# Kernel tuning notes

Measured on AMD Instinct MI355X. Metric: run time of the kernel, lower is better.

## Reference

```python
import jax, jax.numpy as jnp
import numpy as np

B, T, H, W, C = 8, 32, 64, 64, 3
F = 24        # conv filters
U = 128       # lstm units
O = 1         # output units

def _conv(x, w, b):
    # x: [N,H,W,Cin], w: [3,3,Cin,Cout], SAME padding, linear activation
    y = jax.lax.conv_general_dilated(x, w, window_strides=(1, 1), padding='SAME',
                                     dimension_numbers=('NHWC', 'HWIO', 'NHWC'))
    return y + b

def setup_inputs() -> dict:
    key = jax.random.key(0)
    ks = jax.random.split(key, 16)
    s = lambda *shape: 0.05
    inp = {
        'x': jax.random.normal(ks[0], (B, T, H, W, C), dtype=jnp.float32),
        'conv1_w': jax.random.normal(ks[1], (3, 3, C, F), dtype=jnp.float32) * 0.1,
        'conv1_b': jnp.zeros((F,), jnp.float32),
        'conv2_w': jax.random.normal(ks[2], (3, 3, F, F), dtype=jnp.float32) * 0.1,
        'conv2_b': jnp.zeros((F,), jnp.float32),
        'Wf': jax.random.normal(ks[3], (F + U, U), dtype=jnp.float32) * 0.08,
        'bf': jnp.zeros((U,), jnp.float32),
        'Wi': jax.random.normal(ks[4], (F + U, U), dtype=jnp.float32) * 0.08,
        'bi': jnp.zeros((U,), jnp.float32),
        'Wc': jax.random.normal(ks[5], (F + U, U), dtype=jnp.float32) * 0.08,
        'bc': jnp.zeros((U,), jnp.float32),
        'Wo': jax.random.normal(ks[6], (F + U, U), dtype=jnp.float32) * 0.08,
        'bo': jnp.zeros((U,), jnp.float32),
        'out_w': jax.random.normal(ks[7], (U, O), dtype=jnp.float32) * 0.08,
        'out_b': jnp.zeros((O,), jnp.float32),
    }
    return inp

def reference(x, conv1_w, conv1_b, conv2_w, conv2_b, Wf, bf, Wi, bi, Wc, bc, Wo, bo, out_w, out_b):
    b, t, h, w, c = x.shape
    # CNN block (per-frame): two linear 3x3 convs, no pooling inside block
    xr = x.reshape(b * t, h, w, c)
    xr = _conv(xr, conv1_w, conv1_b)
    xr = _conv(xr, conv2_w, conv2_b)
    # TimeDistributed(GlobalAvgPool2D): mean over H,W -> [B,T,F]
    feat = xr.reshape(b, t, h, w, -1).mean(axis=(2, 3))

    # custom LSTM recurrence over time via scan
    def step(carry, xt):
        hs, cs = carry
        z = jnp.concatenate([xt, hs], axis=-1)           # [B, F+U]
        f = jax.nn.sigmoid(z @ Wf + bf)
        i = jax.nn.sigmoid(z @ Wi + bi)
        g = jnp.tanh(z @ Wc + bc)
        o = jax.nn.sigmoid(z @ Wo + bo)
        c_new = cs * f + i * g
        h_new = jnp.tanh(c_new) * o
        return (h_new, c_new), h_new

    h0 = jnp.zeros((b, Wf.shape[1]), x.dtype)
    c0 = jnp.zeros((b, Wf.shape[1]), x.dtype)
    _, hs = jax.lax.scan(step, (h0, c0), jnp.swapaxes(feat, 0, 1))  # [T,B,U]
    hs = jnp.swapaxes(hs, 0, 1)                                     # [B,T,U]
    return hs @ out_w + out_b                                       # [B,T,O]
```

## Files before the change

kernel.cpp:

```cpp
#include <hip/hip_runtime.h>
#include <math.h>

#define Bb 8
#define Tt 32
#define Hh 64
#define Ww 64
#define Cc 3
#define Ff 24
#define Uu 128

typedef float v2f __attribute__((ext_vector_type(2)));

__device__ __forceinline__ float fast_sigmoid(float x) {
    float e = __builtin_amdgcn_exp2f(-1.442695040888963f * x);
    return __builtin_amdgcn_rcpf(1.f + e);
}
__device__ __forceinline__ float fast_tanh(float x) {
    float e = __builtin_amdgcn_exp2f(-2.885390081777927f * x);
    return 2.f * __builtin_amdgcn_rcpf(1.f + e) - 1.f;
}

__global__ void convfeat_kernel(const float* __restrict__ x,
                                const float* __restrict__ w1, const float* __restrict__ b1,
                                const float* __restrict__ w2, const float* __restrict__ b2,
                                const float* __restrict__ Wf, const float* __restrict__ bf,
                                const float* __restrict__ Wi, const float* __restrict__ bi,
                                const float* __restrict__ Wc, const float* __restrict__ bc,
                                const float* __restrict__ Wo, const float* __restrict__ bo,
                                float* __restrict__ G) {
    int n = blockIdx.x;
    const float* xf = x + (size_t)n * (Hh * Ww * Cc);
    int tid  = threadIdx.x;
    int row  = tid >> 2;
    int part = tid & 3;

    __shared__ float partial[256][3];
    __shared__ float rowsum[64][3];
    __shared__ float colv[64][12];
    __shared__ float st[75];
    __shared__ float yst[24][9];
    __shared__ float feats[24];

    float s0 = 0.f, s1 = 0.f, s2 = 0.f;
    const float4* p4 = (const float4*)(xf + (row * Ww + part * 16) * Cc);
#pragma unroll
    for (int i = 0; i < 12; ++i) {
        float4 v = p4[i];
        int j = i * 4;
        float vv[4] = {v.x, v.y, v.z, v.w};
#pragma unroll
        for (int l = 0; l < 4; ++l) {
            int c = (j + l) % 3;
            if (c == 0) s0 += vv[l]; else if (c == 1) s1 += vv[l]; else s2 += vv[l];
        }
    }
    partial[tid][0] = s0; partial[tid][1] = s1; partial[tid][2] = s2;

    if (tid < 64) {
        int r = tid;
#pragma unroll
        for (int w4 = 0; w4 < 4; ++w4) {
            int w = (w4 < 2) ? w4 : 60 + w4;
#pragma unroll
            for (int c = 0; c < 3; ++c) colv[r][w4 * 3 + c] = xf[(r * Ww + w) * Cc + c];
        }
    }
    __syncthreads();

    if (part == 0) {
#pragma unroll
        for (int c = 0; c < 3; ++c)
            rowsum[row][c] = partial[tid][c] + partial[tid + 1][c]
                           + partial[tid + 2][c] + partial[tid + 3][c];
    }
    __syncthreads();

    if (tid < 3) {
        float t = 0.f;
        for (int r = 0; r < 64; ++r) t += rowsum[r][tid];
        st[tid * 25 + 0] = t;
    }
    if (tid >= 4 && tid < 16) {
        int k = tid - 4; int ri = k / 3, c = k % 3;
        int r = (ri < 2) ? ri : 60 + ri;
        st[c * 25 + 1 + ri] = rowsum[r][c];
    }
    if (tid >= 64 && tid < 76) {
        int k = tid - 64;
        float t = 0.f;
        for (int r = 0; r < 64; ++r) t += colv[r][k];
        int wi = k / 3, c = k % 3;
        st[c * 25 + 5 + wi] = t;
    }
    if (tid >= 128 && tid < 176) {
        int k = tid - 128; int pos = k / 3, c = k % 3;
        int ri = pos >> 2, wi = pos & 3;
        int r = (ri < 2) ? ri : 60 + ri;
        int w = (wi < 2) ? wi : 60 + wi;
        st[c * 25 + 9 + pos] = xf[(r * Ww + w) * Cc + c];
    }
    __syncthreads();

    if (tid < 24) {
        int f = tid;
        float Sy = 0, r0 = 0, r63 = 0, c0 = 0, c63 = 0, y00 = 0, y0W = 0, yH0 = 0, yHW = 0;
        for (int c = 0; c < 3; ++c) {
            const float* S = st + c * 25;
            float Sx = S[0];
            float rX[4] = {S[1], S[2], S[3], S[4]};
            float cX[4] = {S[5], S[6], S[7], S[8]};
            const float* X = S + 9;
            #define W1(p, q) w1[(((p) * 3 + (q)) * 3 + c) * 24 + f]
#pragma unroll
            for (int p = 0; p < 3; ++p)
#pragma unroll
                for (int q = 0; q < 3; ++q) {
                    float t = Sx;
                    if (p == 0) t -= rX[3];
                    if (p == 2) t -= rX[0];
                    if (q == 0) t -= cX[3];
                    if (q == 2) t -= cX[0];
                    if (p == 0 && q == 0) t += X[3 * 4 + 3];
                    if (p == 0 && q == 2) t += X[3 * 4 + 0];
                    if (p == 2 && q == 0) t += X[0 * 4 + 3];
                    if (p == 2 && q == 2) t += X[0 * 4 + 0];
                    Sy += W1(p, q) * t;
                }
#pragma unroll
            for (int q = 0; q < 3; ++q) {
                float Rr0  = rX[0] - ((q == 0) ? X[0 * 4 + 3] : 0.f) - ((q == 2) ? X[0 * 4 + 0] : 0.f);
                float Rr1  = rX[1] - ((q == 0) ? X[1 * 4 + 3] : 0.f) - ((q == 2) ? X[1 * 4 + 0] : 0.f);
                float Rr62 = rX[2] - ((q == 0) ? X[2 * 4 + 3] : 0.f) - ((q == 2) ? X[2 * 4 + 0] : 0.f);
                float Rr63 = rX[3] - ((q == 0) ? X[3 * 4 + 3] : 0.f) - ((q == 2) ? X[3 * 4 + 0] : 0.f);
                r0  += W1(1, q) * Rr0  + W1(2, q) * Rr1;
                r63 += W1(0, q) * Rr62 + W1(1, q) * Rr63;
            }
#pragma unroll
            for (int p = 0; p < 3; ++p) {
                float Rc0  = cX[0] - ((p == 0) ? X[3 * 4 + 0] : 0.f) - ((p == 2) ? X[0 * 4 + 0] : 0.f);
                float Rc1  = cX[1] - ((p == 0) ? X[3 * 4 + 1] : 0.f) - ((p == 2) ? X[0 * 4 + 1] : 0.f);
                float Rc62 = cX[2] - ((p == 0) ? X[3 * 4 + 2] : 0.f) - ((p == 2) ? X[0 * 4 + 2] : 0.f);
                float Rc63 = cX[3] - ((p == 0) ? X[3 * 4 + 3] : 0.f) - ((p == 2) ? X[0 * 4 + 3] : 0.f);
                c0  += W1(p, 1) * Rc0  + W1(p, 2) * Rc1;
                c63 += W1(p, 0) * Rc62 + W1(p, 1) * Rc63;
            }
            y00 += W1(1, 1) * X[0 * 4 + 0] + W1(1, 2) * X[0 * 4 + 1]
                 + W1(2, 1) * X[1 * 4 + 0] + W1(2, 2) * X[1 * 4 + 1];
            y0W += W1(1, 0) * X[0 * 4 + 2] + W1(1, 1) * X[0 * 4 + 3]
                 + W1(2, 0) * X[1 * 4 + 2] + W1(2, 1) * X[1 * 4 + 3];
            yH0 += W1(0, 1) * X[2 * 4 + 0] + W1(0, 2) * X[2 * 4 + 1]
                 + W1(1, 1) * X[3 * 4 + 0] + W1(1, 2) * X[3 * 4 + 1];
            yHW += W1(0, 0) * X[2 * 4 + 2] + W1(0, 1) * X[2 * 4 + 3]
                 + W1(1, 0) * X[3 * 4 + 2] + W1(1, 1) * X[3 * 4 + 3];
            #undef W1
        }
        float bb = b1[f];
        yst[f][0] = Sy + 4096.f * bb;
        yst[f][1] = r0 + 64.f * bb;
        yst[f][2] = r63 + 64.f * bb;
        yst[f][3] = c0 + 64.f * bb;
        yst[f][4] = c63 + 64.f * bb;
        yst[f][5] = y00 + bb; yst[f][6] = y0W + bb;
        yst[f][7] = yH0 + bb; yst[f][8] = yHW + bb;
    }
    __syncthreads();

    if (tid < 24) {
        int g = tid;
        float acc = 0.f;
        for (int f = 0; f < 24; ++f) {
            float Sy = yst[f][0], rY0 = yst[f][1], rY63 = yst[f][2], cY0 = yst[f][3], cY63 = yst[f][4];
            float yc00 = yst[f][5], yc0W = yst[f][6], ycH0 = yst[f][7], ycHW = yst[f][8];
#pragma unroll
            for (int p = 0; p < 3; ++p)
#pragma unroll
                for (int q = 0; q < 3; ++q) {
                    float t = Sy;
                    if (p == 0) t -= rY63;
                    if (p == 2) t -= rY0;
                    if (q == 0) t -= cY63;
                    if (q == 2) t -= cY0;
                    if (p == 0 && q == 0) t += ycHW;
                    if (p == 0 && q == 2) t += ycH0;
                    if (p == 2 && q == 0) t += yc0W;
                    if (p == 2 && q == 2) t += yc00;
                    acc += w2[(((p * 3 + q) * 24 + f) * 24) + g] * t;
                }
        }
        feats[g] = b2[g] + acc * (1.f / 4096.f);
    }
    __syncthreads();

    int b = n >> 5, t = n & 31;
    float* Gdst = G + ((size_t)(t * Bb + b)) * 512;
#pragma unroll
    for (int rep = 0; rep < 2; ++rep) {
        int col = tid + rep * 256;
        int gg = col >> 7, u = col & 127;
        const float* W    = (gg == 0) ? Wf : (gg == 1) ? Wi : (gg == 2) ? Wc : Wo;
        const float* bias = (gg == 0) ? bf : (gg == 1) ? bi : (gg == 2) ? bc : bo;
        float acc = bias[u];
#pragma unroll
        for (int k = 0; k < Ff; ++k) acc += feats[k] * W[k * Uu + u];
        Gdst[col] = acc;
    }
}

__global__ __launch_bounds__(1024, 4) void lstm_kernel(
        const float* __restrict__ G,
        const float* __restrict__ Wf, const float* __restrict__ Wi,
        const float* __restrict__ Wc, const float* __restrict__ Wo,
        const float* __restrict__ out_w, const float* __restrict__ out_b,
        float* __restrict__ out) {
    int b   = blockIdx.x;
    int tid = threadIdx.x;
    int up  = tid & 63;
    int g   = (tid >> 6) & 3;
    int q   = tid >> 8;
    const float* Wg = (g == 0) ? Wf : (g == 1) ? Wi : (g == 2) ? Wc : Wo;

    const float* wbase = Wg + (size_t)(Ff + 32 * q) * Uu + 2 * up;
#define LDW(i) v2f w##i = *(const v2f*)(wbase + (size_t)(i) * Uu)
    LDW(0);  LDW(1);  LDW(2);  LDW(3);  LDW(4);  LDW(5);  LDW(6);  LDW(7);
    LDW(8);  LDW(9);  LDW(10); LDW(11); LDW(12); LDW(13); LDW(14); LDW(15);
    LDW(16); LDW(17); LDW(18); LDW(19); LDW(20); LDW(21); LDW(22); LDW(23);
    LDW(24); LDW(25); LDW(26); LDW(27); LDW(28); LDW(29); LDW(30); LDW(31);
#undef LDW
#define KA8(a,b_,c,d,e,f,g_,h) asm volatile("" : "+v"(a),"+v"(b_),"+v"(c),\
        "+v"(d),"+v"(e),"+v"(f),"+v"(g_),"+v"(h))
    KA8(w0,  w1,  w2,  w3,  w4,  w5,  w6,  w7);
    KA8(w8,  w9,  w10, w11, w12, w13, w14, w15);
    KA8(w16, w17, w18, w19, w20, w21, w22, w23);
    KA8(w24, w25, w26, w27, w28, w29, w30, w31);
#undef KA8

    __shared__ float Gl[Tt][512];
    __shared__ float hs[Uu];
    __shared__ float part[16][Uu];
    __shared__ float hist[Tt][Uu];

    {
        int r  = tid >> 5;
        int c0 = (tid & 31) * 16;
        const float4* src = (const float4*)(G + ((size_t)(r * Bb + b)) * 512 + c0);
        float4* dst = (float4*)(&Gl[r][c0]);
#pragma unroll
        for (int i = 0; i < 4; ++i) dst[i] = src[i];
    }

    float cs = 0.f;
    if (tid < Uu) hs[tid] = 0.f;
    __syncthreads();

    for (int t = 0; t < Tt; ++t) {
        v2f ae = {0.f, 0.f}, ao = {0.f, 0.f};
        const v2f* hp = (const v2f*)(hs + q * 32);
#define FMA2(j, we, wo_) { v2f h2 = hp[j]; \
        asm("v_pk_fma_f32 %0, %1, %2, %0 op_sel:[0,0,0] op_sel_hi:[1,0,1]" \
            : "+v"(ae) : "v"(we), "v"(h2)); \
        asm("v_pk_fma_f32 %0, %1, %2, %0 op_sel:[0,1,0] op_sel_hi:[1,1,1]" \
            : "+v"(ao) : "v"(wo_), "v"(h2)); }
        FMA2(0,  w0,  w1);  FMA2(1,  w2,  w3);
        FMA2(2,  w4,  w5);  FMA2(3,  w6,  w7);
        FMA2(4,  w8,  w9);  FMA2(5,  w10, w11);
        FMA2(6,  w12, w13); FMA2(7,  w14, w15);
        FMA2(8,  w16, w17); FMA2(9,  w18, w19);
        FMA2(10, w20, w21); FMA2(11, w22, w23);
        FMA2(12, w24, w25); FMA2(13, w26, w27);
        FMA2(14, w28, w29); FMA2(15, w30, w31);
#undef FMA2
        v2f acc = ae + ao;
        *(v2f*)&part[q * 4 + g][2 * up] = acc;
        __syncthreads();

        if (tid < Uu) {
            int u = tid;
            float sf = part[0][u] + part[4][u] + part[8][u]  + part[12][u] + Gl[t][u];
            float si = part[1][u] + part[5][u] + part[9][u]  + part[13][u] + Gl[t][128 + u];
            float sg = part[2][u] + part[6][u] + part[10][u] + part[14][u] + Gl[t][256 + u];
            float so = part[3][u] + part[7][u] + part[11][u] + part[15][u] + Gl[t][384 + u];
            float f  = fast_sigmoid(sf);
            float i  = fast_sigmoid(si);
            float gg = fast_tanh(sg);
            float o  = fast_sigmoid(so);
            cs = cs * f + i * gg;
            float hn = fast_tanh(cs) * o;
            hs[u] = hn;
            hist[t][u] = hn;
        }
        __syncthreads();
    }

    int tt = tid >> 5, j = tid & 31;
    const float4* hh = (const float4*)(&hist[tt][j * 4]);
    float4 a0 = hh[0];
    const float* owp = out_w + j * 4;
    float pw = a0.x * owp[0] + a0.y * owp[1] + a0.z * owp[2] + a0.w * owp[3];
#pragma unroll
    for (int off = 16; off > 0; off >>= 1) pw += __shfl_down(pw, off, 32);
    if (j == 0) out[b * Tt + tt] = pw + out_b[0];
}

extern "C" void kernel_launch(void* const* d_in, const int* in_sizes, int n_in,
                              void* d_out, int out_size, void* d_ws, size_t ws_size,
                              hipStream_t stream) {
    const float* x   = (const float*)d_in[0];
    const float* w1  = (const float*)d_in[1];
    const float* b1  = (const float*)d_in[2];
    const float* w2  = (const float*)d_in[3];
    const float* b2  = (const float*)d_in[4];
    const float* Wf  = (const float*)d_in[5];
    const float* bf  = (const float*)d_in[6];
    const float* Wi  = (const float*)d_in[7];
    const float* bi  = (const float*)d_in[8];
    const float* Wc  = (const float*)d_in[9];
    const float* bc  = (const float*)d_in[10];
    const float* Wo  = (const float*)d_in[11];
    const float* bo  = (const float*)d_in[12];
    const float* ow  = (const float*)d_in[13];
    const float* ob  = (const float*)d_in[14];
    float* out = (float*)d_out;

    float* G = (float*)d_ws;

    convfeat_kernel<<<Bb * Tt, 256, 0, stream>>>(x, w1, b1, w2, b2,
                                                 Wf, bf, Wi, bi, Wc, bc, Wo, bo, G);
    lstm_kernel<<<Bb, 1024, 0, stream>>>(G, Wf, Wi, Wc, Wo, ow, ob, out);
}
```

Before: 39.66 us.

## Halve LSTM block to 512 threads with four output columns per thread

Result: faster. 38.57 us (-2.7%).

```diff
diff --git a/kernel.cpp b/kernel.cpp
--- a/kernel.cpp
+++ b/kernel.cpp
@@ -206,7 +206,7 @@
     }
 }
 
-__global__ __launch_bounds__(1024, 4) void lstm_kernel(
+__global__ __launch_bounds__(512, 2) void lstm_kernel(
         const float* __restrict__ G,
         const float* __restrict__ Wf, const float* __restrict__ Wi,
         const float* __restrict__ Wc, const float* __restrict__ Wo,
@@ -214,38 +214,40 @@
         float* __restrict__ out) {
     int b   = blockIdx.x;
     int tid = threadIdx.x;
-    int up  = tid & 63;
-    int g   = (tid >> 6) & 3;
-    int q   = tid >> 8;
-    const float* Wg = (g == 0) ? Wf : (g == 1) ? Wi : (g == 2) ? Wc : Wo;
-
-    const float* wbase = Wg + (size_t)(Ff + 32 * q) * Uu + 2 * up;
-#define LDW(i) v2f w##i = *(const v2f*)(wbase + (size_t)(i) * Uu)
+    int cg  = tid & 127;
+    int q   = tid >> 7;
+    int gate = cg >> 5;
+    int c0   = (cg & 31) * 4;
+    const float* Wg = (gate == 0) ? Wf : (gate == 1) ? Wi : (gate == 2) ? Wc : Wo;
+
+    const float* wbase = Wg + (size_t)(Ff + 32 * q) * Uu + c0;
+#define LDW(i) v2f a##i = *(const v2f*)(wbase + (size_t)(i) * Uu); \
+               v2f b##i = *(const v2f*)(wbase + (size_t)(i) * Uu + 2)
     LDW(0);  LDW(1);  LDW(2);  LDW(3);  LDW(4);  LDW(5);  LDW(6);  LDW(7);
     LDW(8);  LDW(9);  LDW(10); LDW(11); LDW(12); LDW(13); LDW(14); LDW(15);
     LDW(16); LDW(17); LDW(18); LDW(19); LDW(20); LDW(21); LDW(22); LDW(23);
     LDW(24); LDW(25); LDW(26); LDW(27); LDW(28); LDW(29); LDW(30); LDW(31);
 #undef LDW
-#define KA8(a,b_,c,d,e,f,g_,h) asm volatile("" : "+v"(a),"+v"(b_),"+v"(c),\
-        "+v"(d),"+v"(e),"+v"(f),"+v"(g_),"+v"(h))
-    KA8(w0,  w1,  w2,  w3,  w4,  w5,  w6,  w7);
-    KA8(w8,  w9,  w10, w11, w12, w13, w14, w15);
-    KA8(w16, w17, w18, w19, w20, w21, w22, w23);
-    KA8(w24, w25, w26, w27, w28, w29, w30, w31);
+#define KA8(p0,p1,p2,p3,p4,p5,p6,p7) asm volatile("" : "+v"(p0),"+v"(p1),\
+        "+v"(p2),"+v"(p3),"+v"(p4),"+v"(p5),"+v"(p6),"+v"(p7))
+    KA8(a0,b0,a1,b1,a2,b2,a3,b3);       KA8(a4,b4,a5,b5,a6,b6,a7,b7);
+    KA8(a8,b8,a9,b9,a10,b10,a11,b11);   KA8(a12,b12,a13,b13,a14,b14,a15,b15);
+    KA8(a16,b16,a17,b17,a18,b18,a19,b19); KA8(a20,b20,a21,b21,a22,b22,a23,b23);
+    KA8(a24,b24,a25,b25,a26,b26,a27,b27); KA8(a28,b28,a29,b29,a30,b30,a31,b31);
 #undef KA8
 
     __shared__ float Gl[Tt][512];
-    __shared__ float hs[Uu];
-    __shared__ float part[16][Uu];
+    __shared__ __align__(16) float hs[Uu];
+    __shared__ float part[4][512];
     __shared__ float hist[Tt][Uu];
 
     {
-        int r  = tid >> 5;
-        int c0 = (tid & 31) * 16;
-        const float4* src = (const float4*)(G + ((size_t)(r * Bb + b)) * 512 + c0);
-        float4* dst = (float4*)(&Gl[r][c0]);
-#pragma unroll
-        for (int i = 0; i < 4; ++i) dst[i] = src[i];
+        int r  = tid >> 4;
+        int cc = (tid & 15) * 32;
+        const float4* src = (const float4*)(G + ((size_t)(r * Bb + b)) * 512 + cc);
+        float4* dst = (float4*)(&Gl[r][cc]);
+#pragma unroll
+        for (int i = 0; i < 8; ++i) dst[i] = src[i];
     }
 
     float cs = 0.f;
@@ -253,32 +255,47 @@
     __syncthreads();
 
     for (int t = 0; t < Tt; ++t) {
-        v2f ae = {0.f, 0.f}, ao = {0.f, 0.f};
-        const v2f* hp = (const v2f*)(hs + q * 32);
-#define FMA2(j, we, wo_) { v2f h2 = hp[j]; \
+        v2f ae0 = {0.f, 0.f}, ao0 = {0.f, 0.f};
+        v2f ae1 = {0.f, 0.f}, ao1 = {0.f, 0.f};
+        const float4* hp = (const float4*)(hs + q * 32);
+#define FMA4(hq, wA0,wB0, wA1,wB1, wA2,wB2, wA3,wB3) { \
+        v2f hlo = {hq.x, hq.y}; v2f hhi = {hq.z, hq.w}; \
         asm("v_pk_fma_f32 %0, %1, %2, %0 op_sel:[0,0,0] op_sel_hi:[1,0,1]" \
-            : "+v"(ae) : "v"(we), "v"(h2)); \
+            : "+v"(ae0) : "v"(wA0), "v"(hlo)); \
+        asm("v_pk_fma_f32 %0, %1, %2, %0 op_sel:[0,0,0] op_sel_hi:[1,0,1]" \
+            : "+v"(ae1) : "v"(wB0), "v"(hlo)); \
         asm("v_pk_fma_f32 %0, %1, %2, %0 op_sel:[0,1,0] op_sel_hi:[1,1,1]" \
-            : "+v"(ao) : "v"(wo_), "v"(h2)); }
-        FMA2(0,  w0,  w1);  FMA2(1,  w2,  w3);
-        FMA2(2,  w4,  w5);  FMA2(3,  w6,  w7);
-        FMA2(4,  w8,  w9);  FMA2(5,  w10, w11);
-        FMA2(6,  w12, w13); FMA2(7,  w14, w15);
-        FMA2(8,  w16, w17); FMA2(9,  w18, w19);
-        FMA2(10, w20, w21); FMA2(11, w22, w23);
-        FMA2(12, w24, w25); FMA2(13, w26, w27);
-        FMA2(14, w28, w29); FMA2(15, w30, w31);
-#undef FMA2
-        v2f acc = ae + ao;
-        *(v2f*)&part[q * 4 + g][2 * up] = acc;
+            : "+v"(ao0) : "v"(wA1), "v"(hlo)); \
+        asm("v_pk_fma_f32 %0, %1, %2, %0 op_sel:[0,1,0] op_sel_hi:[1,1,1]" \
+            : "+v"(ao1) : "v"(wB1), "v"(hlo)); \
+        asm("v_pk_fma_f32 %0, %1, %2, %0 op_sel:[0,0,0] op_sel_hi:[1,0,1]" \
+            : "+v"(ae0) : "v"(wA2), "v"(hhi)); \
+        asm("v_pk_fma_f32 %0, %1, %2, %0 op_sel:[0,0,0] op_sel_hi:[1,0,1]" \
+            : "+v"(ae1) : "v"(wB2), "v"(hhi)); \
+        asm("v_pk_fma_f32 %0, %1, %2, %0 op_sel:[0,1,0] op_sel_hi:[1,1,1]" \
+            : "+v"(ao0) : "v"(wA3), "v"(hhi)); \
+        asm("v_pk_fma_f32 %0, %1, %2, %0 op_sel:[0,1,0] op_sel_hi:[1,1,1]" \
+            : "+v"(ao1) : "v"(wB3), "v"(hhi)); }
+        { float4 h0 = hp[0]; FMA4(h0, a0,b0, a1,b1, a2,b2, a3,b3); }
+        { float4 h1 = hp[1]; FMA4(h1, a4,b4, a5,b5, a6,b6, a7,b7); }
+        { float4 h2 = hp[2]; FMA4(h2, a8,b8, a9,b9, a10,b10, a11,b11); }
+        { float4 h3 = hp[3]; FMA4(h3, a12,b12, a13,b13, a14,b14, a15,b15); }
+        { float4 h4 = hp[4]; FMA4(h4, a16,b16, a17,b17, a18,b18, a19,b19); }
+        { float4 h5 = hp[5]; FMA4(h5, a20,b20, a21,b21, a22,b22, a23,b23); }
+        { float4 h6 = hp[6]; FMA4(h6, a24,b24, a25,b25, a26,b26, a27,b27); }
+        { float4 h7 = hp[7]; FMA4(h7, a28,b28, a29,b29, a30,b30, a31,b31); }
+#undef FMA4
+        v2f s0 = ae0 + ao0, s1 = ae1 + ao1;
+        float4 pw4; pw4.x = s0.x; pw4.y = s0.y; pw4.z = s1.x; pw4.w = s1.y;
+        *(float4*)&part[q][gate * 128 + c0] = pw4;
         __syncthreads();
 
         if (tid < Uu) {
             int u = tid;
-            float sf = part[0][u] + part[4][u] + part[8][u]  + part[12][u] + Gl[t][u];
-            float si = part[1][u] + part[5][u] + part[9][u]  + part[13][u] + Gl[t][128 + u];
-            float sg = part[2][u] + part[6][u] + part[10][u] + part[14][u] + Gl[t][256 + u];
-            float so = part[3][u] + part[7][u] + part[11][u] + part[15][u] + Gl[t][384 + u];
+            float sf = part[0][u]       + part[1][u]       + part[2][u]       + part[3][u]       + Gl[t][u];
+            float si = part[0][128 + u] + part[1][128 + u] + part[2][128 + u] + part[3][128 + u] + Gl[t][128 + u];
+            float sg = part[0][256 + u] + part[1][256 + u] + part[2][256 + u] + part[3][256 + u] + Gl[t][256 + u];
+            float so = part[0][384 + u] + part[1][384 + u] + part[2][384 + u] + part[3][384 + u] + Gl[t][384 + u];
             float f  = fast_sigmoid(sf);
             float i  = fast_sigmoid(si);
             float gg = fast_tanh(sg);
@@ -291,13 +308,14 @@
         __syncthreads();
     }
 
-    int tt = tid >> 5, j = tid & 31;
-    const float4* hh = (const float4*)(&hist[tt][j * 4]);
-    float4 a0 = hh[0];
-    const float* owp = out_w + j * 4;
-    float pw = a0.x * owp[0] + a0.y * owp[1] + a0.z * owp[2] + a0.w * owp[3];
-#pragma unroll
-    for (int off = 16; off > 0; off >>= 1) pw += __shfl_down(pw, off, 32);
+    int tt = tid >> 4, j = tid & 15;
+    const float4* hh = (const float4*)(&hist[tt][j * 8]);
+    float4 a0q = hh[0], a1q = hh[1];
+    const float* owp = out_w + j * 8;
+    float pw = a0q.x * owp[0] + a0q.y * owp[1] + a0q.z * owp[2] + a0q.w * owp[3]
+             + a1q.x * owp[4] + a1q.y * owp[5] + a1q.z * owp[6] + a1q.w * owp[7];
+#pragma unroll
+    for (int off = 8; off > 0; off >>= 1) pw += __shfl_down(pw, off, 16);
     if (j == 0) out[b * Tt + tt] = pw + out_b[0];
 }
 
@@ -325,5 +343,5 @@
 
     convfeat_kernel<<<Bb * Tt, 256, 0, stream>>>(x, w1, b1, w2, b2,
                                                  Wf, bf, Wi, bi, Wc, bc, Wo, bo, G);
-    lstm_kernel<<<Bb, 1024, 0, stream>>>(G, Wf, Wi, Wc, Wo, ow, ob, out);
-}
+    lstm_kernel<<<Bb, 512, 0, stream>>>(G, Wf, Wi, Wc, Wo, ow, ob, out);
+}
```

## Remap LSTM work so gate reduction stays in-wavefront, one barrier per step

Applied to the files above, without the earlier changes.

After: 52.78 us. +33.1%, slower.

```diff
diff --git a/kernel.cpp b/kernel.cpp
--- a/kernel.cpp
+++ b/kernel.cpp
@@ -214,78 +214,75 @@
         float* __restrict__ out) {
     int b   = blockIdx.x;
     int tid = threadIdx.x;
-    int up  = tid & 63;
-    int g   = (tid >> 6) & 3;
-    int q   = tid >> 8;
+    int w   = tid >> 6;
+    int l   = tid & 63;
+    int k   = l >> 5;
+    int g   = (l >> 3) & 3;
+    int uj  = l & 7;
+    int u   = 8 * w + uj;
     const float* Wg = (g == 0) ? Wf : (g == 1) ? Wi : (g == 2) ? Wc : Wo;
 
-    const float* wbase = Wg + (size_t)(Ff + 32 * q) * Uu + 2 * up;
-#define LDW(i) v2f w##i = *(const v2f*)(wbase + (size_t)(i) * Uu)
+    const float* wb = Wg + (size_t)(Ff + 64 * k) * Uu + u;
+#define LDW(i) v2f w##i = { wb[(2*(i)) * Uu], wb[(2*(i)+1) * Uu] }
     LDW(0);  LDW(1);  LDW(2);  LDW(3);  LDW(4);  LDW(5);  LDW(6);  LDW(7);
     LDW(8);  LDW(9);  LDW(10); LDW(11); LDW(12); LDW(13); LDW(14); LDW(15);
     LDW(16); LDW(17); LDW(18); LDW(19); LDW(20); LDW(21); LDW(22); LDW(23);
     LDW(24); LDW(25); LDW(26); LDW(27); LDW(28); LDW(29); LDW(30); LDW(31);
 #undef LDW
-#define KA8(a,b_,c,d,e,f,g_,h) asm volatile("" : "+v"(a),"+v"(b_),"+v"(c),\
-        "+v"(d),"+v"(e),"+v"(f),"+v"(g_),"+v"(h))
-    KA8(w0,  w1,  w2,  w3,  w4,  w5,  w6,  w7);
-    KA8(w8,  w9,  w10, w11, w12, w13, w14, w15);
-    KA8(w16, w17, w18, w19, w20, w21, w22, w23);
-    KA8(w24, w25, w26, w27, w28, w29, w30, w31);
+#define KA8(p0,p1,p2,p3,p4,p5,p6,p7) asm volatile("" : "+v"(p0),"+v"(p1),\
+        "+v"(p2),"+v"(p3),"+v"(p4),"+v"(p5),"+v"(p6),"+v"(p7))
+    KA8(w0,w1,w2,w3,w4,w5,w6,w7);         KA8(w8,w9,w10,w11,w12,w13,w14,w15);
+    KA8(w16,w17,w18,w19,w20,w21,w22,w23); KA8(w24,w25,w26,w27,w28,w29,w30,w31);
 #undef KA8
 
     __shared__ float Gl[Tt][512];
-    __shared__ float hs[Uu];
-    __shared__ float part[16][Uu];
+    __shared__ float hsb[2][Uu];
     __shared__ float hist[Tt][Uu];
 
     {
         int r  = tid >> 5;
-        int c0 = (tid & 31) * 16;
-        const float4* src = (const float4*)(G + ((size_t)(r * Bb + b)) * 512 + c0);
-        float4* dst = (float4*)(&Gl[r][c0]);
-#pragma unroll
-        for (int i = 0; i < 4; ++i) dst[i] = src[i];
-    }
-
+        int cc = (tid & 31) * 16;
+        const float4* src = (const float4*)(G + ((size_t)(r * Bb + b)) * 512 + cc);
+        float4* dst = (float4*)(&Gl[r][cc]);
+        dst[0] = src[0]; dst[1] = src[1]; dst[2] = src[2]; dst[3] = src[3];
+    }
+    if (tid < Uu) hsb[0][tid] = 0.f;
     float cs = 0.f;
-    if (tid < Uu) hs[tid] = 0.f;
-    __syncthreads();
-
+    __syncthreads();
+
+#pragma clang loop unroll(disable)
     for (int t = 0; t < Tt; ++t) {
-        v2f ae = {0.f, 0.f}, ao = {0.f, 0.f};
-        const v2f* hp = (const v2f*)(hs + q * 32);
-#define FMA2(j, we, wo_) { v2f h2 = hp[j]; \
-        asm("v_pk_fma_f32 %0, %1, %2, %0 op_sel:[0,0,0] op_sel_hi:[1,0,1]" \
-            : "+v"(ae) : "v"(we), "v"(h2)); \
-        asm("v_pk_fma_f32 %0, %1, %2, %0 op_sel:[0,1,0] op_sel_hi:[1,1,1]" \
-            : "+v"(ao) : "v"(wo_), "v"(h2)); }
-        FMA2(0,  w0,  w1);  FMA2(1,  w2,  w3);
-        FMA2(2,  w4,  w5);  FMA2(3,  w6,  w7);
-        FMA2(4,  w8,  w9);  FMA2(5,  w10, w11);
-        FMA2(6,  w12, w13); FMA2(7,  w14, w15);
-        FMA2(8,  w16, w17); FMA2(9,  w18, w19);
-        FMA2(10, w20, w21); FMA2(11, w22, w23);
-        FMA2(12, w24, w25); FMA2(13, w26, w27);
-        FMA2(14, w28, w29); FMA2(15, w30, w31);
-#undef FMA2
-        v2f acc = ae + ao;
-        *(v2f*)&part[q * 4 + g][2 * up] = acc;
-        __syncthreads();
-
-        if (tid < Uu) {
-            int u = tid;
-            float sf = part[0][u] + part[4][u] + part[8][u]  + part[12][u] + Gl[t][u];
-            float si = part[1][u] + part[5][u] + part[9][u]  + part[13][u] + Gl[t][128 + u];
-            float sg = part[2][u] + part[6][u] + part[10][u] + part[14][u] + Gl[t][256 + u];
-            float so = part[3][u] + part[7][u] + part[11][u] + part[15][u] + Gl[t][384 + u];
-            float f  = fast_sigmoid(sf);
-            float i  = fast_sigmoid(si);
-            float gg = fast_tanh(sg);
-            float o  = fast_sigmoid(so);
-            cs = cs * f + i * gg;
-            float hn = fast_tanh(cs) * o;
-            hs[u] = hn;
+        const float* hr = hsb[t & 1];
+        const float4* hp = (const float4*)(hr + 64 * k);
+        v2f accA = {0.f, 0.f}, accB = {0.f, 0.f};
+#define ST4(i, wE, wO) { float4 h4 = hp[i]; \
+        v2f hlo = {h4.x, h4.y}, hhi = {h4.z, h4.w}; \
+        asm("v_pk_fma_f32 %0, %1, %2, %0" : "+v"(accA) : "v"(wE), "v"(hlo)); \
+        asm("v_pk_fma_f32 %0, %1, %2, %0" : "+v"(accB) : "v"(wO), "v"(hhi)); }
+        ST4(0,  w0,  w1);  ST4(1,  w2,  w3);  ST4(2,  w4,  w5);
+        ST4(3,  w6,  w7);  ST4(4,  w8,  w9);  ST4(5,  w10, w11);
+        ST4(6,  w12, w13); ST4(7,  w14, w15); ST4(8,  w16, w17);
+        ST4(9,  w18, w19); ST4(10, w20, w21); ST4(11, w22, w23);
+        ST4(12, w24, w25); ST4(13, w26, w27); ST4(14, w28, w29);
+        ST4(15, w30, w31);
+#undef ST4
+        float s = (accA.x + accA.y) + (accB.x + accB.y);
+        float full = s + __shfl_xor(s, 32);
+        float vi = __shfl(full, 8 + uj);
+        float vg = __shfl(full, 16 + uj);
+        float vo = __shfl(full, 24 + uj);
+        float sf = full + Gl[t][u];
+        float si = vi + Gl[t][128 + u];
+        float sg = vg + Gl[t][256 + u];
+        float so = vo + Gl[t][384 + u];
+        float ff  = fast_sigmoid(sf);
+        float ii  = fast_sigmoid(si);
+        float g3  = fast_tanh(sg);
+        float o3  = fast_sigmoid(so);
+        cs = cs * ff + ii * g3;
+        float hn = fast_tanh(cs) * o3;
+        if (l < 8) {
+            hsb[(t + 1) & 1][u] = hn;
             hist[t][u] = hn;
         }
         __syncthreads();
@@ -293,9 +290,9 @@
 
     int tt = tid >> 5, j = tid & 31;
     const float4* hh = (const float4*)(&hist[tt][j * 4]);
-    float4 a0 = hh[0];
+    float4 a0q = hh[0];
     const float* owp = out_w + j * 4;
-    float pw = a0.x * owp[0] + a0.y * owp[1] + a0.z * owp[2] + a0.w * owp[3];
+    float pw = a0q.x * owp[0] + a0q.y * owp[1] + a0q.z * owp[2] + a0q.w * owp[3];
 #pragma unroll
     for (int off = 16; off > 0; off >>= 1) pw += __shfl_down(pw, off, 32);
     if (j == 0) out[b * Tt + tt] = pw + out_b[0];
```
